# Performance work log

Hardware: AMD Instinct MI355X
Metric: run time of the kernel (lower is better)

## Reference

```python
import jax, jax.numpy as jnp
import numpy as np

BN_EPS = 1e-3
SLOPE = 0.1
K = 100
CLUSTER_TEMP = 5.0


def setup_inputs() -> dict:
    key = jax.random.key(0)
    ks = jax.random.split(key, 5)
    N, Cin, Cout = 8192, 1, 64
    d = 49 * Cout  # (28/4)^2 * out_channels
    return {
        "x": jax.random.normal(ks[0], (N, Cin, 28, 28), jnp.float32),
        "conv1_w": jax.random.normal(ks[1], (128, Cin, 5, 5), jnp.float32) * 0.05,
        "conv1_b": jnp.zeros((128,), jnp.float32),
        "bn1_gamma": jnp.ones((128,), jnp.float32),
        "bn1_beta": jnp.zeros((128,), jnp.float32),
        "bn1_mean": jnp.zeros((128,), jnp.float32),
        "bn1_var": jnp.ones((128,), jnp.float32),
        "conv2_w": jax.random.normal(ks[2], (Cout, 128, 5, 5), jnp.float32) * 0.02,
        "conv2_b": jnp.zeros((Cout,), jnp.float32),
        "bn2_gamma": jnp.ones((Cout,), jnp.float32),
        "bn2_beta": jnp.zeros((Cout,), jnp.float32),
        "bn2_mean": jnp.zeros((Cout,), jnp.float32),
        "bn2_var": jnp.ones((Cout,), jnp.float32),
        "init_mu": jax.random.uniform(ks[3], (K, d), jnp.float32),
        "num_iter": 10,
    }


def _conv_bn_lrelu(x, w, b, gamma, beta, mean, var):
    # Conv2d(k=5, s=2, p=2) -> BatchNorm (eval/running stats) -> LeakyReLU(0.1)
    h = jax.lax.conv_general_dilated(
        x, w, window_strides=(2, 2), padding=[(2, 2), (2, 2)],
        dimension_numbers=("NCHW", "OIHW", "NCHW"))
    h = h + b[None, :, None, None]
    inv = gamma * jax.lax.rsqrt(var + BN_EPS)
    h = h * inv[None, :, None, None] + (beta - mean * inv)[None, :, None, None]
    return jnp.where(h >= 0, h, SLOPE * h)


def _cluster(data, mu, num_iter):
    # Row L2-normalize (equivalent to diag(1/||row||) @ data)
    data = data / jnp.linalg.norm(data, axis=1, keepdims=True)  # [n, d]
    for _ in range(num_iter):
        dist = data @ mu.T                                 # [n, K]
        r = jax.nn.softmax(CLUSTER_TEMP * dist, axis=1)    # [n, K]
        cluster_r = r.sum(axis=0)                          # [K]
        cluster_mean = r.T @ data                          # [K, d]
        mu = cluster_mean / cluster_r[:, None]
    dist = data @ mu.T
    r = jax.nn.softmax(CLUSTER_TEMP * dist, axis=1)
    return mu, r, dist


def reference(x, conv1_w, conv1_b, bn1_gamma, bn1_beta, bn1_mean, bn1_var,
              conv2_w, conv2_b, bn2_gamma, bn2_beta, bn2_mean, bn2_var,
              init_mu, num_iter):
    h = _conv_bn_lrelu(x, conv1_w, conv1_b, bn1_gamma, bn1_beta, bn1_mean, bn1_var)
    h = _conv_bn_lrelu(h, conv2_w, conv2_b, bn2_gamma, bn2_beta, bn2_mean, bn2_var)
    embeds = h.reshape(h.shape[0], -1)                     # [N, 49*Cout]
    mu_init, _, _ = _cluster(embeds, init_mu, int(num_iter))
    mu, r, dist = _cluster(embeds, jax.lax.stop_gradient(mu_init), 1)
    return mu, r, dist
```

## Files before the change

kernel.cpp:

```cpp
#include <hip/hip_runtime.h>
#include <hip/hip_bf16.h>
#include <math.h>

#define BN_EPS 1e-3f
#define SLOPE  0.1f
#define TEMP   5.0f
#define DDIM   3136

typedef __attribute__((ext_vector_type(8))) short bf16x8;
typedef __attribute__((ext_vector_type(4))) float f32x4;

#define W2T_OFF   0u
#define W2T_SZ    (3200u*64u)
#define DB_OFF    (W2T_OFF + W2T_SZ)
#define DB_SZ     (8192u*3136u/2u)
#define DT_OFF    (DB_OFF + DB_SZ)
#define DT_SZ     (8192u*3136u/2u)
#define MUB_OFF   (DT_OFF + DT_SZ)
#define MUB_SZ    (112u*3136u/2u)
#define MUF_OFF   (MUB_OFF + MUB_SZ)
#define MUF_SZ    (100u*3136u)
#define CMT_OFF   (MUF_OFF + MUF_SZ)
#define CMT_SZ    (3136u*112u)
#define RT_OFF    (CMT_OFF + CMT_SZ)
#define RT_SZ     (112u*8192u/2u)
#define CR_OFF    (RT_OFF + RT_SZ)

__global__ __launch_bounds__(256) void k_w2b(const float* __restrict__ w2,
                                             __hip_bfloat16* __restrict__ w2b) {
  int idx = blockIdx.x * 256 + threadIdx.x;
  if (idx >= 204800) return;
  int ci   = idx & 31;
  int lr   = (idx >> 5) & 15;
  int rest = idx >> 9;
  int kk   = rest % 100;
  int oct  = rest / 100;
  int oc   = oct * 16 + lr;
  int tap  = kk >> 2;
  int c    = ((kk & 3) << 5) + ci;
  w2b[idx] = __float2bfloat16(w2[(oc * 128 + c) * 25 + tap]);
}

__global__ __launch_bounds__(256) void k_conv(
    const float* __restrict__ x,
    const float* __restrict__ w1,  const float* __restrict__ b1,
    const float* __restrict__ g1,  const float* __restrict__ be1,
    const float* __restrict__ mn1, const float* __restrict__ vr1,
    const __hip_bfloat16* __restrict__ w2bh, const float* __restrict__ b2,
    const float* __restrict__ g2,  const float* __restrict__ be2,
    const float* __restrict__ mn2, const float* __restrict__ vr2,
    __hip_bfloat16* __restrict__ db) {
  __shared__ float xs[1024];
  __shared__ float bn2s[128];
  __shared__ float nrm[4];
  __shared__ __align__(16) __hip_bfloat16 h1s[197 * 128];

  const int t    = threadIdx.x;
  const int img  = blockIdx.x;
  const int lane = t & 63;
  const int wv   = t >> 6;
  const int lr   = lane & 15;
  const int kg   = lane >> 4;
  const short* w2b = (const short*)w2bh;

  for (int i = t; i < 1024; i += 256) xs[i] = 0.f;
  if (t < 64) {
    float a2 = g2[t] * rsqrtf(vr2[t] + BN_EPS);
    bn2s[t]      = a2;
    bn2s[64 + t] = b2[t] * a2 + be2[t] - mn2[t] * a2;
    ((unsigned*)(h1s + 196 * 128))[t] = 0u;
  }
  __syncthreads();
  const float* xi = x + (size_t)img * 784;
  for (int i = t; i < 784; i += 256) {
    int yy = i / 28, xx = i % 28;
    xs[(yy + 2) * 32 + (xx + 2)] = xi[i];
  }
  __syncthreads();

  {
    const int c = t & 127;
    const int h = t >> 7;
    float wr[25];
#pragma unroll
    for (int tap = 0; tap < 25; ++tap) wr[tap] = w1[c * 25 + tap];
    const float a1 = g1[c] * rsqrtf(vr1[c] + BN_EPS);
    const float s1 = b1[c] * a1 + be1[c] - mn1[c] * a1;
    const int swzc = c * 2;
    for (int oy = 0; oy < 14; ++oy) {
#pragma unroll
      for (int j = 0; j < 7; ++j) {
        const int ox = 2 * j + h;
        const float* xb = xs + (2 * oy) * 32 + 2 * ox;
        float accv = 0.f;
#pragma unroll
        for (int kh = 0; kh < 5; ++kh)
#pragma unroll
          for (int kw = 0; kw < 5; ++kw)
            accv += xb[kh * 32 + kw] * wr[kh * 5 + kw];
        float hv = accv * a1 + s1;
        hv = (hv >= 0.f) ? hv : SLOPE * hv;
        const int pxy = oy * 14 + ox;
        *(__hip_bfloat16*)((char*)h1s + pxy * 256 + (swzc ^ ((pxy & 7) << 4))) =
            __float2bfloat16(hv);
      }
    }
  }
  __syncthreads();

  const int woff  = lr * 32 + kg * 8;
  const int kgoff = kg << 4;
  int pxA[4], oyA[4], oxA[4];
#pragma unroll
  for (int pt = 0; pt < 4; ++pt) {
    int p = pt * 16 + lr;
    pxA[pt] = p;
    oyA[pt] = p / 7;
    oxA[pt] = p - 7 * oyA[pt];
  }

  f32x4 acc[4][4];
#pragma unroll
  for (int oct = 0; oct < 4; ++oct)
#pragma unroll
    for (int pt = 0; pt < 4; ++pt) acc[oct][pt] = (f32x4){0.f, 0.f, 0.f, 0.f};

  const int s0 = 25 * wv, s1e = s0 + 25;
  int curtap = -1;
  int rowB[4], rowS[4];

  auto loadk = [&](int kk, bf16x8* areg, bf16x8* breg) {
    int tap = kk >> 2;
    if (tap != curtap) {
      curtap = tap;
      int kh = tap / 5, kw = tap - 5 * (tap / 5);
#pragma unroll
      for (int pt = 0; pt < 4; ++pt) {
        int iy = 2 * oyA[pt] - 2 + kh;
        int ix = 2 * oxA[pt] - 2 + kw;
        bool val = (pxA[pt] < 49) & ((unsigned)iy < 14u) & ((unsigned)ix < 14u);
        int ip = val ? iy * 14 + ix : 196;
        rowB[pt] = ip * 256;
        rowS[pt] = (ip & 7) << 4;
      }
    }
    int c01 = (kk & 3) << 6;
#pragma unroll
    for (int oct = 0; oct < 4; ++oct)
      areg[oct] = *(const bf16x8*)(w2b + ((oct * 100 + kk) << 9) + woff);
#pragma unroll
    for (int pt = 0; pt < 4; ++pt)
      breg[pt] = *(const bf16x8*)((const char*)h1s + rowB[pt] +
                                  ((c01 | kgoff) ^ rowS[pt]));
  };

  bf16x8 a[4], b[4], an[4], bn[4];
  loadk(s0, a, b);
  for (int kk = s0; kk < s1e; ++kk) {
    if (kk + 1 < s1e) loadk(kk + 1, an, bn);
#pragma unroll
    for (int oct = 0; oct < 4; ++oct)
#pragma unroll
      for (int pt = 0; pt < 4; ++pt)
        acc[oct][pt] = __builtin_amdgcn_mfma_f32_16x16x32_bf16(a[oct], b[pt],
                                                               acc[oct][pt], 0, 0, 0);
#pragma unroll
    for (int q = 0; q < 4; ++q) { a[q] = an[q]; b[q] = bn[q]; }
  }
  __syncthreads();

  float* red = (float*)h1s;
  if (wv != 0) {
#pragma unroll
    for (int oct = 0; oct < 4; ++oct)
#pragma unroll
      for (int pt = 0; pt < 4; ++pt)
#pragma unroll
        for (int r = 0; r < 4; ++r)
          red[(wv - 1) * 4096 + ((oct * 4 + pt) * 4 + r) * 64 + lane] =
              acc[oct][pt][r];
  }
  __syncthreads();
  if (wv == 0) {
#pragma unroll
    for (int oct = 0; oct < 4; ++oct)
#pragma unroll
      for (int pt = 0; pt < 4; ++pt)
#pragma unroll
        for (int r = 0; r < 4; ++r) {
          const int i = (oct * 4 + pt) * 4 + r;
          float v = acc[oct][pt][r] + red[i * 64 + lane] +
                    red[4096 + i * 64 + lane] + red[8192 + i * 64 + lane];
          red[i * 64 + lane] = v;
        }
  }
  __syncthreads();

  float outv[16];
  float ss = 0.f;
#pragma unroll
  for (int pt = 0; pt < 4; ++pt) {
#pragma unroll
    for (int r = 0; r < 4; ++r) {
      const int i = ((wv * 4 + pt) * 4 + r);
      float v = red[i * 64 + lane];
      const int oc = wv * 16 + kg * 4 + r;
      v = v * bn2s[oc] + bn2s[64 + oc];
      v = (v >= 0.f) ? v : SLOPE * v;
      outv[pt * 4 + r] = v;
      if (pxA[pt] < 49) ss += v * v;
    }
  }
#pragma unroll
  for (int m = 1; m < 64; m <<= 1) ss += __shfl_xor(ss, m, 64);
  if (lane == 0) nrm[wv] = ss;
  __syncthreads();
  const float invn = rsqrtf(nrm[0] + nrm[1] + nrm[2] + nrm[3]);
  __hip_bfloat16* dro = db + (size_t)img * DDIM;
#pragma unroll
  for (int pt = 0; pt < 4; ++pt) {
    if (pxA[pt] < 49) {
#pragma unroll
      for (int r = 0; r < 4; ++r) {
        const int oc = wv * 16 + kg * 4 + r;
        dro[oc * 49 + pxA[pt]] = __float2bfloat16(outv[pt * 4 + r] * invn);
      }
    }
  }
}

__global__ __launch_bounds__(256) void k_tr(const __hip_bfloat16* __restrict__ dbh,
                                            __hip_bfloat16* __restrict__ dTh) {
  __shared__ short tile[64][72];
  const int t   = threadIdx.x;
  const int i   = t >> 2;
  const int seg = t & 3;
  const size_t img0 = (size_t)blockIdx.x * 64;
  const size_t d0   = (size_t)blockIdx.y * 64;
  const short* src = (const short*)dbh + (img0 + i) * DDIM + d0 + seg * 16;
  bf16x8 v0 = *(const bf16x8*)src;
  bf16x8 v1 = *(const bf16x8*)(src + 8);
  *(bf16x8*)&tile[i][seg * 16]     = v0;
  *(bf16x8*)&tile[i][seg * 16 + 8] = v1;
  __syncthreads();
  short tmp[16];
#pragma unroll
  for (int k = 0; k < 16; ++k) tmp[k] = tile[seg * 16 + k][i];
  short* dst = (short*)dTh + (d0 + i) * 8192 + img0 + seg * 16;
  *(bf16x8*)dst       = *(bf16x8*)tmp;
  *(bf16x8*)(dst + 8) = *((bf16x8*)tmp + 1);
}

__global__ __launch_bounds__(256) void k_muinit(const float* __restrict__ mu0,
                                                __hip_bfloat16* __restrict__ mub) {
  int idx = blockIdx.x * 256 + threadIdx.x;
  if (idx >= 112 * DDIM) return;
  int j = idx / DDIM, d = idx - j * DDIM;
  float v = (j < 100) ? mu0[j * DDIM + d] : 0.f;
  mub[idx] = __float2bfloat16(v);
}

__global__ __launch_bounds__(256) void k_dsm(
    const __hip_bfloat16* __restrict__ data,
    const __hip_bfloat16* __restrict__ mu,
    __hip_bfloat16* __restrict__ rT,
    float* __restrict__ cr,
    float* __restrict__ outr,
    float* __restrict__ outd,
    int final_flag) {
  __shared__ float red[3][64][28];
  const int t    = threadIdx.x;
  const int lane = t & 63;
  const int wv   = t >> 6;
  const int rowbase = blockIdx.x * 16;
  const int s0 = (98 * wv) >> 2;
  const int s1 = (98 * (wv + 1)) >> 2;
  const int lr = lane & 15;
  const int kg = lane >> 4;

  const __hip_bfloat16* arow = data + (size_t)(rowbase + lr) * DDIM + kg * 8;
  const __hip_bfloat16* brow = mu + (size_t)lr * DDIM + kg * 8;

  f32x4 acc[7];
#pragma unroll
  for (int i = 0; i < 7; ++i) acc[i] = (f32x4){0.f, 0.f, 0.f, 0.f};

  for (int s = s0; s < s1; ++s) {
    const int k0 = s * 32;
    bf16x8 a = *(const bf16x8*)(arow + k0);
#pragma unroll
    for (int tl = 0; tl < 7; ++tl) {
      bf16x8 b = *(const bf16x8*)(brow + (size_t)tl * 16 * DDIM + k0);
      acc[tl] = __builtin_amdgcn_mfma_f32_16x16x32_bf16(a, b, acc[tl], 0, 0, 0);
    }
  }

  if (wv != 0) {
#pragma unroll
    for (int tl = 0; tl < 7; ++tl)
#pragma unroll
      for (int r = 0; r < 4; ++r) red[wv - 1][lane][tl * 4 + r] = acc[tl][r];
  }
  __syncthreads();
  if (wv != 0) return;

#pragma unroll
  for (int tl = 0; tl < 7; ++tl)
#pragma unroll
    for (int r = 0; r < 4; ++r)
      acc[tl][r] += red[0][lane][tl * 4 + r] + red[1][lane][tl * 4 + r] +
                    red[2][lane][tl * 4 + r];

  if (final_flag) {
#pragma unroll
    for (int tl = 0; tl < 7; ++tl) {
      const int col = tl * 16 + lr;
      if (col < 100) {
#pragma unroll
        for (int r = 0; r < 4; ++r)
          outd[(size_t)(rowbase + kg * 4 + r) * 100 + col] = acc[tl][r];
      }
    }
  }

#pragma unroll
  for (int r = 0; r < 4; ++r) {
    float m = -1e30f;
#pragma unroll
    for (int tl = 0; tl < 7; ++tl) {
      const bool valid = (tl < 6) || (lr < 4);
      m = fmaxf(m, valid ? acc[tl][r] : -1e30f);
    }
    m = fmaxf(m, __shfl_xor(m, 1, 64));
    m = fmaxf(m, __shfl_xor(m, 2, 64));
    m = fmaxf(m, __shfl_xor(m, 4, 64));
    m = fmaxf(m, __shfl_xor(m, 8, 64));
    float s = 0.f;
    float e[7];
#pragma unroll
    for (int tl = 0; tl < 7; ++tl) {
      const bool valid = (tl < 6) || (lr < 4);
      e[tl] = valid ? __expf(TEMP * (acc[tl][r] - m)) : 0.f;
      s += e[tl];
    }
    s += __shfl_xor(s, 1, 64);
    s += __shfl_xor(s, 2, 64);
    s += __shfl_xor(s, 4, 64);
    s += __shfl_xor(s, 8, 64);
    const float inv = 1.f / s;
#pragma unroll
    for (int tl = 0; tl < 7; ++tl) acc[tl][r] = e[tl] * inv;
  }

  if (final_flag) {
#pragma unroll
    for (int tl = 0; tl < 7; ++tl) {
      const int col = tl * 16 + lr;
      if (col < 100) {
#pragma unroll
        for (int r = 0; r < 4; ++r)
          outr[(size_t)(rowbase + kg * 4 + r) * 100 + col] = acc[tl][r];
      }
    }
    return;
  }

#pragma unroll
  for (int tl = 0; tl < 7; ++tl) {
    const int col = tl * 16 + lr;
    if (col < 100) {
#pragma unroll
      for (int r = 0; r < 4; ++r)
        rT[(size_t)col * 8192 + rowbase + kg * 4 + r] = __float2bfloat16(acc[tl][r]);
    }
  }
  float csum[7];
#pragma unroll
  for (int tl = 0; tl < 7; ++tl) {
    float cs = acc[tl][0] + acc[tl][1] + acc[tl][2] + acc[tl][3];
    cs += __shfl_xor(cs, 16, 64);
    cs += __shfl_xor(cs, 32, 64);
    csum[tl] = cs;
  }
  if (lane < 16) {
#pragma unroll
    for (int tl = 0; tl < 7; ++tl) {
      const int col = tl * 16 + lane;
      if (col < 100) atomicAdd(cr + col, csum[tl]);
    }
  }
}

__global__ __launch_bounds__(256) void k_mu(
    const __hip_bfloat16* __restrict__ dataT,
    const __hip_bfloat16* __restrict__ rT,
    float* __restrict__ cmeanT) {
  const int t    = threadIdx.x;
  const int lane = t & 63;
  const int wv   = t >> 6;
  const int mbase = blockIdx.x * 64 + wv * 16;
  const int kbase = blockIdx.y * 1024;
  const int lr = lane & 15;
  const int kg = lane >> 4;

  const __hip_bfloat16* arow = dataT + (size_t)(mbase + lr) * 8192 + kbase + kg * 8;
  const __hip_bfloat16* brow = rT + (size_t)lr * 8192 + kbase + kg * 8;

  f32x4 acc[7];
#pragma unroll
  for (int i = 0; i < 7; ++i) acc[i] = (f32x4){0.f, 0.f, 0.f, 0.f};

  for (int s = 0; s < 32; ++s) {
    const int k0 = s * 32;
    bf16x8 a = *(const bf16x8*)(arow + k0);
#pragma unroll
    for (int tl = 0; tl < 7; ++tl) {
      bf16x8 b = *(const bf16x8*)(brow + (size_t)tl * 16 * 8192 + k0);
      acc[tl] = __builtin_amdgcn_mfma_f32_16x16x32_bf16(a, b, acc[tl], 0, 0, 0);
    }
  }

#pragma unroll
  for (int tl = 0; tl < 7; ++tl) {
    const int col = tl * 16 + lr;
    if (col < 100) {
#pragma unroll
      for (int r = 0; r < 4; ++r)
        atomicAdd(cmeanT + (size_t)(mbase + kg * 4 + r) * 112 + col, acc[tl][r]);
    }
  }
}

__global__ __launch_bounds__(256) void k_upd(const float* __restrict__ cmeanT,
                                             const float* __restrict__ cr,
                                             float* __restrict__ muf,
                                             __hip_bfloat16* __restrict__ mub) {
  int idx = blockIdx.x * 256 + threadIdx.x;
  if (idx >= 100 * DDIM) return;
  int j = idx / DDIM, d = idx - j * DDIM;
  float v = cmeanT[(size_t)d * 112 + j] / cr[j];
  muf[idx] = v;
  mub[idx] = __float2bfloat16(v);
}

extern "C" void kernel_launch(void* const* d_in, const int* in_sizes, int n_in,
                              void* d_out, int out_size, void* d_ws, size_t ws_size,
                              hipStream_t stream) {
  const float* x   = (const float*)d_in[0];
  const float* w1  = (const float*)d_in[1];
  const float* b1  = (const float*)d_in[2];
  const float* g1  = (const float*)d_in[3];
  const float* be1 = (const float*)d_in[4];
  const float* mn1 = (const float*)d_in[5];
  const float* vr1 = (const float*)d_in[6];
  const float* w2  = (const float*)d_in[7];
  const float* b2  = (const float*)d_in[8];
  const float* g2  = (const float*)d_in[9];
  const float* be2 = (const float*)d_in[10];
  const float* mn2 = (const float*)d_in[11];
  const float* vr2 = (const float*)d_in[12];
  const float* mu0 = (const float*)d_in[13];

  float* ws = (float*)d_ws;
  __hip_bfloat16* w2b = (__hip_bfloat16*)(ws + W2T_OFF);
  __hip_bfloat16* db  = (__hip_bfloat16*)(ws + DB_OFF);
  __hip_bfloat16* dT  = (__hip_bfloat16*)(ws + DT_OFF);
  __hip_bfloat16* mub = (__hip_bfloat16*)(ws + MUB_OFF);
  float*          muf = ws + MUF_OFF;
  float*          cmt = ws + CMT_OFF;
  __hip_bfloat16* rT  = (__hip_bfloat16*)(ws + RT_OFF);
  float*          cr  = ws + CR_OFF;
  float*          out = (float*)d_out;

  k_w2b<<<800, 256, 0, stream>>>(w2, w2b);
  k_conv<<<8192, 256, 0, stream>>>(x, w1, b1, g1, be1, mn1, vr1,
                                   w2b, b2, g2, be2, mn2, vr2, db);
  k_tr<<<dim3(128, 49), 256, 0, stream>>>(db, dT);
  k_muinit<<<(112 * DDIM + 255) / 256, 256, 0, stream>>>(mu0, mub);
  hipMemsetAsync(rT + (size_t)100 * 8192, 0, 12 * 8192 * sizeof(__hip_bfloat16),
                 stream);

  for (int it = 0; it < 11; ++it) {
    hipMemsetAsync(cr, 0, 128 * sizeof(float), stream);
    hipMemsetAsync(cmt, 0, (size_t)CMT_SZ * sizeof(float), stream);
    k_dsm<<<512, 256, 0, stream>>>(db, mub, rT, cr, nullptr, nullptr, 0);
    k_mu<<<dim3(49, 8), 256, 0, stream>>>(dT, rT, cmt);
    k_upd<<<(100 * DDIM + 255) / 256, 256, 0, stream>>>(cmt, cr, muf, mub);
  }

  k_dsm<<<512, 256, 0, stream>>>(db, mub, rT, cr, out + 313600, out + 1132800, 1);
  hipMemcpyAsync(out, muf, (size_t)MUF_SZ * sizeof(float),
                 hipMemcpyDeviceToDevice, stream);
}
```

Baseline: 1.999 ms.

## Run conv1 on MFMA, prefetch GEMM operands, replace atomics with split-K partial buffers

```diff
diff --git a/kernel.cpp b/kernel.cpp
--- a/kernel.cpp
+++ b/kernel.cpp
@@ -10,9 +10,14 @@
 typedef __attribute__((ext_vector_type(8))) short bf16x8;
 typedef __attribute__((ext_vector_type(4))) float f32x4;
 
-#define W2T_OFF   0u
-#define W2T_SZ    (3200u*64u)
-#define DB_OFF    (W2T_OFF + W2T_SZ)
+static __device__ __forceinline__ short f2b(float f) {
+  __hip_bfloat16 h = __float2bfloat16(f);
+  return *reinterpret_cast<short*>(&h);
+}
+
+#define W2B_OFF   0u
+#define W1B_OFF   102400u
+#define DB_OFF    204800u
 #define DB_SZ     (8192u*3136u/2u)
 #define DT_OFF    (DB_OFF + DB_SZ)
 #define DT_SZ     (8192u*3136u/2u)
@@ -20,9 +25,9 @@
 #define MUB_SZ    (112u*3136u/2u)
 #define MUF_OFF   (MUB_OFF + MUB_SZ)
 #define MUF_SZ    (100u*3136u)
-#define CMT_OFF   (MUF_OFF + MUF_SZ)
-#define CMT_SZ    (3136u*112u)
-#define RT_OFF    (CMT_OFF + CMT_SZ)
+#define CMS_OFF   (MUF_OFF + MUF_SZ)
+#define CMS_SZ    (8u*3136u*112u)
+#define RT_OFF    (CMS_OFF + CMS_SZ)
 #define RT_SZ     (112u*8192u/2u)
 #define CR_OFF    (RT_OFF + RT_SZ)
 
@@ -41,9 +46,21 @@
   w2b[idx] = __float2bfloat16(w2[(oc * 128 + c) * 25 + tap]);
 }
 
+__global__ __launch_bounds__(256) void k_w1b(const float* __restrict__ w1,
+                                             __hip_bfloat16* __restrict__ w1b) {
+  int idx = blockIdx.x * 256 + threadIdx.x;
+  if (idx >= 4096) return;
+  int k   = idx & 31;
+  int lr  = (idx >> 5) & 15;
+  int oct = idx >> 9;
+  int oc  = oct * 16 + lr;
+  float v = (k < 25) ? w1[oc * 25 + k] : 0.f;
+  w1b[idx] = __float2bfloat16(v);
+}
+
 __global__ __launch_bounds__(256) void k_conv(
     const float* __restrict__ x,
-    const float* __restrict__ w1,  const float* __restrict__ b1,
+    const __hip_bfloat16* __restrict__ w1bh, const float* __restrict__ b1,
     const float* __restrict__ g1,  const float* __restrict__ be1,
     const float* __restrict__ mn1, const float* __restrict__ vr1,
     const __hip_bfloat16* __restrict__ w2bh, const float* __restrict__ b2,
@@ -52,6 +69,7 @@
     __hip_bfloat16* __restrict__ db) {
   __shared__ float xs[1024];
   __shared__ float bn2s[128];
+  __shared__ float bn1a[128], bn1b[128];
   __shared__ float nrm[4];
   __shared__ __align__(16) __hip_bfloat16 h1s[197 * 128];
 
@@ -62,6 +80,7 @@
   const int lr   = lane & 15;
   const int kg   = lane >> 4;
   const short* w2b = (const short*)w2bh;
+  const short* w1b = (const short*)w1bh;
 
   for (int i = t; i < 1024; i += 256) xs[i] = 0.f;
   if (t < 64) {
@@ -70,6 +89,11 @@
     bn2s[64 + t] = b2[t] * a2 + be2[t] - mn2[t] * a2;
     ((unsigned*)(h1s + 196 * 128))[t] = 0u;
   }
+  if (t < 128) {
+    float a1 = g1[t] * rsqrtf(vr1[t] + BN_EPS);
+    bn1a[t] = a1;
+    bn1b[t] = b1[t] * a1 + be1[t] - mn1[t] * a1;
+  }
   __syncthreads();
   const float* xi = x + (size_t)img * 784;
   for (int i = t; i < 784; i += 256) {
@@ -79,30 +103,55 @@
   __syncthreads();
 
   {
-    const int c = t & 127;
-    const int h = t >> 7;
-    float wr[25];
-#pragma unroll
-    for (int tap = 0; tap < 25; ++tap) wr[tap] = w1[c * 25 + tap];
-    const float a1 = g1[c] * rsqrtf(vr1[c] + BN_EPS);
-    const float s1 = b1[c] * a1 + be1[c] - mn1[c] * a1;
-    const int swzc = c * 2;
-    for (int oy = 0; oy < 14; ++oy) {
-#pragma unroll
-      for (int j = 0; j < 7; ++j) {
-        const int ox = 2 * j + h;
-        const float* xb = xs + (2 * oy) * 32 + 2 * ox;
-        float accv = 0.f;
-#pragma unroll
-        for (int kh = 0; kh < 5; ++kh)
-#pragma unroll
-          for (int kw = 0; kw < 5; ++kw)
-            accv += xb[kh * 32 + kw] * wr[kh * 5 + kw];
-        float hv = accv * a1 + s1;
-        hv = (hv >= 0.f) ? hv : SLOPE * hv;
-        const int pxy = oy * 14 + ox;
-        *(__hip_bfloat16*)((char*)h1s + pxy * 256 + (swzc ^ ((pxy & 7) << 4))) =
-            __float2bfloat16(hv);
+    bf16x8 a0 = *(const bf16x8*)(w1b + (2 * wv) * 512 + lr * 32 + kg * 8);
+    bf16x8 a1 = *(const bf16x8*)(w1b + (2 * wv + 1) * 512 + lr * 32 + kg * 8);
+    for (int pt = 0; pt < 13; ++pt) {
+      const int px  = pt * 16 + lr;
+      const int pxc = (px < 196) ? px : 195;
+      const int oy  = pxc / 14, ox = pxc - 14 * (pxc / 14);
+      const float* xb = xs + (2 * oy) * 32 + 2 * ox;
+      short bs[8];
+#pragma unroll
+      for (int j = 0; j < 8; ++j) {
+        int k   = kg * 8 + j;
+        int tap = (k < 25) ? k : 0;
+        int kh  = tap / 5, kw = tap - 5 * (tap / 5);
+        bs[j] = f2b(xb[kh * 32 + kw]);
+      }
+      bf16x8 b;
+#pragma unroll
+      for (int j = 0; j < 8; ++j) b[j] = bs[j];
+      f32x4 c0 = {0.f, 0.f, 0.f, 0.f}, c1 = {0.f, 0.f, 0.f, 0.f};
+      c0 = __builtin_amdgcn_mfma_f32_16x16x32_bf16(a0, b, c0, 0, 0, 0);
+      c1 = __builtin_amdgcn_mfma_f32_16x16x32_bf16(a1, b, c1, 0, 0, 0);
+      if (px < 196) {
+        const int swz = (px & 7) << 4;
+        unsigned w0lo, w0hi, w1lo, w1hi;
+        {
+          float v[4], u[4];
+#pragma unroll
+          for (int r = 0; r < 4; ++r) {
+            int oc = wv * 32 + kg * 4 + r;
+            float h = c0[r] * bn1a[oc] + bn1b[oc];
+            v[r] = (h >= 0.f) ? h : SLOPE * h;
+            int oc2 = oc + 16;
+            float h2 = c1[r] * bn1a[oc2] + bn1b[oc2];
+            u[r] = (h2 >= 0.f) ? h2 : SLOPE * h2;
+          }
+          w0lo = (unsigned)(unsigned short)f2b(v[0]) |
+                 ((unsigned)(unsigned short)f2b(v[1]) << 16);
+          w0hi = (unsigned)(unsigned short)f2b(v[2]) |
+                 ((unsigned)(unsigned short)f2b(v[3]) << 16);
+          w1lo = (unsigned)(unsigned short)f2b(u[0]) |
+                 ((unsigned)(unsigned short)f2b(u[1]) << 16);
+          w1hi = (unsigned)(unsigned short)f2b(u[2]) |
+                 ((unsigned)(unsigned short)f2b(u[3]) << 16);
+        }
+        char* base = (char*)h1s + px * 256;
+        const int o0 = ((wv * 32 + kg * 4) * 2) ^ swz;
+        const int o1 = ((wv * 32 + 16 + kg * 4) * 2) ^ swz;
+        *(uint2*)(base + o0) = make_uint2(w0lo, w0hi);
+        *(uint2*)(base + o1) = make_uint2(w1lo, w1hi);
       }
     }
   }
@@ -154,10 +203,10 @@
                                   ((c01 | kgoff) ^ rowS[pt]));
   };
 
-  bf16x8 a[4], b[4], an[4], bn[4];
+  bf16x8 a[4], b[4], an[4], bn_[4];
   loadk(s0, a, b);
   for (int kk = s0; kk < s1e; ++kk) {
-    if (kk + 1 < s1e) loadk(kk + 1, an, bn);
+    if (kk + 1 < s1e) loadk(kk + 1, an, bn_);
 #pragma unroll
     for (int oct = 0; oct < 4; ++oct)
 #pragma unroll
@@ -165,7 +214,7 @@
         acc[oct][pt] = __builtin_amdgcn_mfma_f32_16x16x32_bf16(a[oct], b[pt],
                                                                acc[oct][pt], 0, 0, 0);
 #pragma unroll
-    for (int q = 0; q < 4; ++q) { a[q] = an[q]; b[q] = bn[q]; }
+    for (int q = 0; q < 4; ++q) { a[q] = an[q]; b[q] = bn_[q]; }
   }
   __syncthreads();
 
@@ -285,14 +334,28 @@
 #pragma unroll
   for (int i = 0; i < 7; ++i) acc[i] = (f32x4){0.f, 0.f, 0.f, 0.f};
 
+  bf16x8 a, b[7], an, bn_[7];
+  {
+    const int k0 = s0 * 32;
+    a = *(const bf16x8*)(arow + k0);
+#pragma unroll
+    for (int tl = 0; tl < 7; ++tl)
+      b[tl] = *(const bf16x8*)(brow + (size_t)tl * 16 * DDIM + k0);
+  }
   for (int s = s0; s < s1; ++s) {
-    const int k0 = s * 32;
-    bf16x8 a = *(const bf16x8*)(arow + k0);
-#pragma unroll
-    for (int tl = 0; tl < 7; ++tl) {
-      bf16x8 b = *(const bf16x8*)(brow + (size_t)tl * 16 * DDIM + k0);
-      acc[tl] = __builtin_amdgcn_mfma_f32_16x16x32_bf16(a, b, acc[tl], 0, 0, 0);
-    }
+    if (s + 1 < s1) {
+      const int k1 = (s + 1) * 32;
+      an = *(const bf16x8*)(arow + k1);
+#pragma unroll
+      for (int tl = 0; tl < 7; ++tl)
+        bn_[tl] = *(const bf16x8*)(brow + (size_t)tl * 16 * DDIM + k1);
+    }
+#pragma unroll
+    for (int tl = 0; tl < 7; ++tl)
+      acc[tl] = __builtin_amdgcn_mfma_f32_16x16x32_bf16(a, b[tl], acc[tl], 0, 0, 0);
+    a = an;
+#pragma unroll
+    for (int tl = 0; tl < 7; ++tl) b[tl] = bn_[tl];
   }
 
   if (wv != 0) {
@@ -394,7 +457,7 @@
 __global__ __launch_bounds__(256) void k_mu(
     const __hip_bfloat16* __restrict__ dataT,
     const __hip_bfloat16* __restrict__ rT,
-    float* __restrict__ cmeanT) {
+    float* __restrict__ cms) {
   const int t    = threadIdx.x;
   const int lane = t & 63;
   const int wv   = t >> 6;
@@ -410,35 +473,49 @@
 #pragma unroll
   for (int i = 0; i < 7; ++i) acc[i] = (f32x4){0.f, 0.f, 0.f, 0.f};
 
+  bf16x8 a, b[7], an, bn_[7];
+  a = *(const bf16x8*)(arow);
+#pragma unroll
+  for (int tl = 0; tl < 7; ++tl)
+    b[tl] = *(const bf16x8*)(brow + (size_t)tl * 16 * 8192);
   for (int s = 0; s < 32; ++s) {
-    const int k0 = s * 32;
-    bf16x8 a = *(const bf16x8*)(arow + k0);
-#pragma unroll
-    for (int tl = 0; tl < 7; ++tl) {
-      bf16x8 b = *(const bf16x8*)(brow + (size_t)tl * 16 * 8192 + k0);
-      acc[tl] = __builtin_amdgcn_mfma_f32_16x16x32_bf16(a, b, acc[tl], 0, 0, 0);
-    }
-  }
-
+    if (s + 1 < 32) {
+      const int k1 = (s + 1) * 32;
+      an = *(const bf16x8*)(arow + k1);
+#pragma unroll
+      for (int tl = 0; tl < 7; ++tl)
+        bn_[tl] = *(const bf16x8*)(brow + (size_t)tl * 16 * 8192 + k1);
+    }
+#pragma unroll
+    for (int tl = 0; tl < 7; ++tl)
+      acc[tl] = __builtin_amdgcn_mfma_f32_16x16x32_bf16(a, b[tl], acc[tl], 0, 0, 0);
+    a = an;
+#pragma unroll
+    for (int tl = 0; tl < 7; ++tl) b[tl] = bn_[tl];
+  }
+
+  float* dst = cms + (size_t)blockIdx.y * (3136u * 112u);
 #pragma unroll
   for (int tl = 0; tl < 7; ++tl) {
     const int col = tl * 16 + lr;
-    if (col < 100) {
-#pragma unroll
-      for (int r = 0; r < 4; ++r)
-        atomicAdd(cmeanT + (size_t)(mbase + kg * 4 + r) * 112 + col, acc[tl][r]);
-    }
-  }
-}
-
-__global__ __launch_bounds__(256) void k_upd(const float* __restrict__ cmeanT,
+#pragma unroll
+    for (int r = 0; r < 4; ++r)
+      dst[(size_t)(mbase + kg * 4 + r) * 112 + col] = acc[tl][r];
+  }
+}
+
+__global__ __launch_bounds__(256) void k_upd(const float* __restrict__ cms,
                                              const float* __restrict__ cr,
                                              float* __restrict__ muf,
                                              __hip_bfloat16* __restrict__ mub) {
   int idx = blockIdx.x * 256 + threadIdx.x;
   if (idx >= 100 * DDIM) return;
   int j = idx / DDIM, d = idx - j * DDIM;
-  float v = cmeanT[(size_t)d * 112 + j] / cr[j];
+  float v = 0.f;
+#pragma unroll
+  for (int s = 0; s < 8; ++s)
+    v += cms[(size_t)s * (3136u * 112u) + (size_t)d * 112 + j];
+  v /= cr[j];
   muf[idx] = v;
   mub[idx] = __float2bfloat16(v);
 }
@@ -462,18 +539,20 @@
   const float* mu0 = (const float*)d_in[13];
 
   float* ws = (float*)d_ws;
-  __hip_bfloat16* w2b = (__hip_bfloat16*)(ws + W2T_OFF);
+  __hip_bfloat16* w2b = (__hip_bfloat16*)(ws + W2B_OFF);
+  __hip_bfloat16* w1b = (__hip_bfloat16*)(ws + W1B_OFF);
   __hip_bfloat16* db  = (__hip_bfloat16*)(ws + DB_OFF);
   __hip_bfloat16* dT  = (__hip_bfloat16*)(ws + DT_OFF);
   __hip_bfloat16* mub = (__hip_bfloat16*)(ws + MUB_OFF);
   float*          muf = ws + MUF_OFF;
-  float*          cmt = ws + CMT_OFF;
+  float*          cms = ws + CMS_OFF;
   __hip_bfloat16* rT  = (__hip_bfloat16*)(ws + RT_OFF);
   float*          cr  = ws + CR_OFF;
   float*          out = (float*)d_out;
 
   k_w2b<<<800, 256, 0, stream>>>(w2, w2b);
-  k_conv<<<8192, 256, 0, stream>>>(x, w1, b1, g1, be1, mn1, vr1,
+  k_w1b<<<16, 256, 0, stream>>>(w1, w1b);
+  k_conv<<<8192, 256, 0, stream>>>(x, w1b, b1, g1, be1, mn1, vr1,
                                    w2b, b2, g2, be2, mn2, vr2, db);
   k_tr<<<dim3(128, 49), 256, 0, stream>>>(db, dT);
   k_muinit<<<(112 * DDIM + 255) / 256, 256, 0, stream>>>(mu0, mub);
@@ -482,10 +561,9 @@
 
   for (int it = 0; it < 11; ++it) {
     hipMemsetAsync(cr, 0, 128 * sizeof(float), stream);
-    hipMemsetAsync(cmt, 0, (size_t)CMT_SZ * sizeof(float), stream);
     k_dsm<<<512, 256, 0, stream>>>(db, mub, rT, cr, nullptr, nullptr, 0);
-    k_mu<<<dim3(49, 8), 256, 0, stream>>>(dT, rT, cmt);
-    k_upd<<<(100 * DDIM + 255) / 256, 256, 0, stream>>>(cmt, cr, muf, mub);
+    k_mu<<<dim3(49, 8), 256, 0, stream>>>(dT, rT, cms);
+    k_upd<<<(100 * DDIM + 255) / 256, 256, 0, stream>>>(cms, cr, muf, mub);
   }
 
   k_dsm<<<512, 256, 0, stream>>>(db, mub, rT, cr, out + 313600, out + 1132800, 1);
```

Measured after the change: 1.891 ms. 1.06x faster.
